# Optimization experiments

Measured on AMD Instinct MI355X. Metric: run time of the kernel, lower is better.

## Reference

```python
import jax, jax.numpy as jnp
import numpy as np

N_HIDDEN = 2048
D_IN = 64
T_STEPS = 4096
WASHOUT = 200
SPECTRAL_RADIUS = 0.9
RIDGE_LAMBDA = 1e-6


def _scale_to_spectral_radius(W, rho, iters=100):
    # power iteration to estimate the dominant eigenvalue magnitude (spectral radius)
    rng = np.random.default_rng(0)
    v = rng.normal(size=W.shape[0]).astype(np.float64)
    v /= np.linalg.norm(v)
    for _ in range(iters):
        w = W @ v
        nrm = np.linalg.norm(w)
        v = w / nrm
    rad = np.linalg.norm(W @ v)
    return W * (rho / rad)


def setup_inputs() -> dict:
    key = jax.random.key(0)
    k1, k2, k3, k4 = jax.random.split(key, 4)
    u = jax.random.normal(k1, (T_STEPS, D_IN), dtype=jnp.float32)
    y = jax.random.normal(k2, (T_STEPS, 1), dtype=jnp.float32)
    W_in = jax.random.normal(k3, (N_HIDDEN, D_IN), dtype=jnp.float32) * 0.1
    W = np.asarray(jax.random.normal(k4, (N_HIDDEN, N_HIDDEN), dtype=jnp.float32), dtype=np.float64)
    W /= np.sqrt(N_HIDDEN)
    W = _scale_to_spectral_radius(W, SPECTRAL_RADIUS)
    W_res = jnp.asarray(W, dtype=jnp.float32)
    return {"u": u, "y": y, "W_in": W_in, "W_res": W_res, "washout": WASHOUT}


def reference(u, y, W_in, W_res, washout):
    # precompute input drive W_in @ u[t] for all t: [T, N]
    drive = u @ W_in.T
    x0 = jnp.zeros((W_res.shape[0],), dtype=u.dtype)

    def step(x, d):
        x = jnp.tanh(W_res @ x + d)
        return x, x

    _, X = jax.lax.scan(step, x0, drive)  # X: [T, N]
    Xw = X[washout:]                      # [T - washout, N]
    yw = y[washout:]                      # [T - washout, 1]
    A = Xw.T @ Xw + RIDGE_LAMBDA * jnp.eye(Xw.shape[1], dtype=Xw.dtype)
    Wout = jnp.linalg.solve(A, Xw.T @ yw)  # [N, 1]
    return Xw @ Wout                       # [T - washout, 1]
```

## Files before the change

### kernel.cpp

```cpp
#include <hip/hip_runtime.h>
#include <math.h>

#define NH      2048
#define TT      4096
#define DIN     64
#define WASH    200
#define TW      (TT - WASH)
#define LAMBDA  1e-6f

#define CG_BLOCKS    64
#define CG_ITERS     320
#define NTILE        528
#define NWORK        192

typedef unsigned long long u64;

#define X_OFF      ((size_t)0)
#define DRIVE_OFF  ((size_t)TT * NH)
#define A_OFF      DRIVE_OFF
#define B_OFF      ((size_t)2 * TT * NH)
#define INVD_OFF   (B_OFF + NH)
#define XV_OFF     (INVD_OFF + NH)
#define WS_FLOATS  (XV_OFF + NH)
#define XPACK_OFF  ((size_t)0)
#define ZPACK_OFF  ((size_t)2 * NH)
#define PQSLOT_OFF ((size_t)3 * NH)
#define RZSLOT_OFF ((size_t)3 * NH + 64)
#define U64_TOTAL  ((size_t)3 * NH + 128)

__device__ __forceinline__ u64 pack_ev(int epoch, float v) {
    return ((u64)(unsigned)epoch << 32) | (u64)__float_as_uint(v);
}
__device__ __forceinline__ int   ep_of(u64 p)  { return (int)(p >> 32); }
__device__ __forceinline__ float val_of(u64 p) { return __uint_as_float((unsigned)p); }
__device__ __forceinline__ u64 pack2f(float lo, float hi) {
    return ((u64)__float_as_uint(hi) << 32) | (u64)__float_as_uint(lo);
}
__device__ __forceinline__ float lo_of(u64 p) { return __uint_as_float((unsigned)p); }
__device__ __forceinline__ float hi_of(u64 p) { return __uint_as_float((unsigned)(p >> 32)); }

__device__ __forceinline__ u64 aload(const u64* p) {
    return __hip_atomic_load(p, __ATOMIC_RELAXED, __HIP_MEMORY_SCOPE_AGENT);
}
__device__ __forceinline__ void astore(u64* p, u64 v) {
    __hip_atomic_store(p, v, __ATOMIC_RELAXED, __HIP_MEMORY_SCOPE_AGENT);
}

__global__ void init_kernel(float* ws) {
    int tid = threadIdx.x;
    u64* ub = (u64*)(ws + WS_FLOATS);
    for (size_t i = tid; i < U64_TOTAL; i += 256) ub[i] = 0ull;
    for (int i = tid; i < NH; i += 256) ws[B_OFF + i] = 0.f;
}

__global__ __launch_bounds__(256) void drive_kernel(
    const float* __restrict__ u, const float* __restrict__ Win,
    float* __restrict__ drive)
{
    __shared__ float Wt[256 * 64];
    const int tid = threadIdx.x;
    const int ic = blockIdx.x & 7;
    const int tc = blockIdx.x >> 3;
    const int i0 = ic * 256;
    for (int idx = tid; idx < 256 * 64; idx += 256) {
        int il = idx >> 6, k = idx & 63;
        Wt[k * 256 + il] = Win[(size_t)i0 * 64 + idx];
    }
    __syncthreads();
    for (int tt_ = 0; tt_ < 128; ++tt_) {
        int t = tc * 128 + tt_;
        const float* ur = u + (size_t)t * DIN;
        float acc = 0.f;
        #pragma unroll
        for (int k = 0; k < 64; ++k)
            acc = fmaf(Wt[k * 256 + tid], ur[k], acc);
        drive[(size_t)t * NH + i0 + tid] = acc;
    }
}

__global__ __launch_bounds__(1024, 1) void scan_gram_kernel(
    const float* __restrict__ W, const float* __restrict__ drive,
    float* __restrict__ X, u64* xpack, float* __restrict__ A)
{
    __shared__ float xls[NH];
    __shared__ float As[16][64];
    __shared__ float Bs[16][64];
    const int tid = threadIdx.x;

    if (blockIdx.x < 64) {
        const int wave = tid >> 6;
        const int lane = tid & 63;
        const int rowA = blockIdx.x * 32 + wave * 2;

        float4 wA[8], wB[8];
        {
            const float* wpA = W + (size_t)rowA * NH + lane * 4;
            const float* wpB = wpA + NH;
            #pragma unroll
            for (int j = 0; j < 8; ++j) {
                wA[j] = *(const float4*)(wpA + 256 * j);
                wB[j] = *(const float4*)(wpB + 256 * j);
            }
        }

        for (int t = 0; t < TT; ++t) {
            float2 dv = {0.f, 0.f};
            if (lane == 0) dv = *(const float2*)&drive[(size_t)t * NH + rowA];

            if (t == 0) {
                xls[tid] = 0.f; xls[tid + 1024] = 0.f;
            } else {
                const u64* src = xpack + (size_t)((t - 1) & 1) * NH;
                const int want = t;
                u64 a = aload(&src[tid]);
                u64 b = aload(&src[tid + 1024]);
                bool pa = true, pb = true;
                if (ep_of(a) >= want) { xls[tid] = val_of(a); pa = false; }
                if (ep_of(b) >= want) { xls[tid + 1024] = val_of(b); pb = false; }
                while (pa || pb) {
                    __builtin_amdgcn_s_sleep(1);
                    if (pa) { u64 v = aload(&src[tid]);
                              if (ep_of(v) >= want) { xls[tid] = val_of(v); pa = false; } }
                    if (pb) { u64 v = aload(&src[tid + 1024]);
                              if (ep_of(v) >= want) { xls[tid + 1024] = val_of(v); pb = false; } }
                }
            }
            __syncthreads();

            float a0 = 0.f, a1 = 0.f;
            #pragma unroll
            for (int j = 0; j < 8; ++j) {
                float4 xv = *(const float4*)&xls[lane * 4 + 256 * j];
                float4 va = wA[j], vb = wB[j];
                a0 = fmaf(va.x, xv.x, fmaf(va.y, xv.y, fmaf(va.z, xv.z, fmaf(va.w, xv.w, a0))));
                a1 = fmaf(vb.x, xv.x, fmaf(vb.y, xv.y, fmaf(vb.z, xv.z, fmaf(vb.w, xv.w, a1))));
            }
            #pragma unroll
            for (int m = 32; m; m >>= 1) { a0 += __shfl_xor(a0, m); a1 += __shfl_xor(a1, m); }

            if (lane == 0) {
                float v0 = tanhf(a0 + dv.x);
                float v1 = tanhf(a1 + dv.y);
                astore((u64*)&X[(size_t)t * NH + rowA], pack2f(v0, v1));
                u64* dst = xpack + (size_t)(t & 1) * NH;
                astore(&dst[rowA],     pack_ev(t + 1, v0));
                astore(&dst[rowA + 1], pack_ev(t + 1, v1));
            }
            __syncthreads();
        }
        __threadfence();
        if (lane == 0) {
            u64* dst = xpack + (size_t)(TT & 1) * NH;
            astore(&dst[rowA],     pack_ev(TT + 1, 0.f));
            astore(&dst[rowA + 1], pack_ev(TT + 1, 0.f));
        }
    } else {
        const int wid = blockIdx.x - 64;
        int ti0[3], tj0[3]; int nt = 0;
        for (int L = wid; L < NTILE; L += NWORK) {
            int rem = L, a = 0;
            while (rem >= 32 - a) { rem -= 32 - a; ++a; }
            ti0[nt] = a * 64; tj0[nt] = (a + rem) * 64; ++nt;
        }
        float4 acc4[3] = {};
        const int ty = tid >> 5, tx = tid & 31;
        const u64* Xp = (const u64*)X;

        const int nch = (TW + 15) / 16;
        for (int ch = 0; ch < nch; ++ch) {
            const int tb = WASH + ch * 16;
            const int te = (tb + 15 < TT) ? tb + 15 : TT - 1;
            const int want = te + 2;
            const u64* buf = xpack + (size_t)((te + 1) & 1) * NH;
            if (tid < nt * 128) {
                int tt_ = tid >> 7, local = tid & 127;
                int base = (local & 64) ? tj0[tt_] : ti0[tt_];
                int r = base + (local & 63);
                u64 v = aload(&buf[r]);
                while (ep_of(v) < want) { __builtin_amdgcn_s_sleep(64); v = aload(&buf[r]); }
            }
            __syncthreads();

            for (int tt_ = 0; tt_ < nt; ++tt_) {
                const int i0 = ti0[tt_], j0 = tj0[tt_];
                {
                    int v = tid & 511;
                    int kk = v >> 5, c2 = v & 31;
                    int t = tb + kk;
                    int base = (tid < 512) ? i0 : j0;
                    float lo = 0.f, hi = 0.f;
                    if (t < TT) {
                        u64 w_ = aload(&Xp[((size_t)t * NH + base) / 2 + c2]);
                        lo = lo_of(w_); hi = hi_of(w_);
                    }
                    float* Sh = (tid < 512) ? &As[kk][c2 * 2] : &Bs[kk][c2 * 2];
                    Sh[0] = lo; Sh[1] = hi;
                }
                __syncthreads();
                float4 a = acc4[tt_];
                #pragma unroll
                for (int k = 0; k < 16; ++k) {
                    float2 av = *(const float2*)&As[k][ty * 2];
                    float2 bv = *(const float2*)&Bs[k][tx * 2];
                    a.x = fmaf(av.x, bv.x, a.x); a.y = fmaf(av.x, bv.y, a.y);
                    a.z = fmaf(av.y, bv.x, a.z); a.w = fmaf(av.y, bv.y, a.w);
                }
                acc4[tt_] = a;
                __syncthreads();
            }
        }
        for (int tt_ = 0; tt_ < nt; ++tt_) {
            const int i0 = ti0[tt_], j0 = tj0[tt_];
            const bool diag = (i0 == j0);
            float4 a = acc4[tt_];
            float vals[2][2] = {{a.x, a.y}, {a.z, a.w}};
            #pragma unroll
            for (int aa = 0; aa < 2; ++aa) {
                int gi = i0 + ty * 2 + aa;
                #pragma unroll
                for (int bb = 0; bb < 2; ++bb) {
                    int gj = j0 + tx * 2 + bb;
                    float v = vals[aa][bb];
                    if (gi == gj) v += LAMBDA;
                    A[(size_t)gi * NH + gj] = v;
                    if (!diag) A[(size_t)gj * NH + gi] = v;
                }
            }
        }
    }
}

__global__ void bvec_kernel(const float* __restrict__ X, const float* __restrict__ y,
                            float* __restrict__ bv)
{
    const int ic = blockIdx.x & 7, tc = blockIdx.x >> 3;
    const int i = ic * 256 + threadIdx.x;
    const int t0 = WASH + tc * (TW / 8), t1 = t0 + (TW / 8);
    float acc = 0.f;
    for (int t = t0; t < t1; ++t)
        acc = fmaf(X[(size_t)t * NH + i], y[t], acc);
    atomicAdd(&bv[i], acc);
}

__global__ void invdiag_kernel(const float* __restrict__ A, float* __restrict__ invd)
{
    int i = blockIdx.x * 256 + threadIdx.x;
    invd[i] = 1.0f / A[(size_t)i * NH + i];
}

__global__ __launch_bounds__(1024, 1) void cg_kernel(
    const float* __restrict__ A, const float* __restrict__ bvec,
    const float* __restrict__ invd, float* __restrict__ xv,
    u64* zpack, u64* pqslot, u64* rzslot)
{
    __shared__ float pls[NH];
    __shared__ float zls[NH];
    __shared__ float r32[32], x32[32], q32[32], inv32[32];
    __shared__ float csh[2];
    const int tid     = threadIdx.x;
    const int r_local = tid >> 5;
    const int lane32  = tid & 31;
    const int row0 = blockIdx.x * 32;
    const int row  = row0 + r_local;

    float4 areg[16];
    {
        const float* ap = A + (size_t)row * NH + lane32 * 4;
        #pragma unroll
        for (int j = 0; j < 16; ++j) areg[j] = *(const float4*)(ap + 128 * j);
    }

    pls[tid] = 0.f; pls[tid + 1024] = 0.f;

    if (tid < 32) {
        int i = row0 + tid;
        float bi = bvec[i], iv = invd[i];
        inv32[tid] = iv;
        x32[tid] = 0.f; r32[tid] = bi;
        float zi = iv * bi;
        astore(&zpack[i], pack_ev(1, zi));
        float part = bi * zi;
        #pragma unroll
        for (int m = 16; m; m >>= 1) part += __shfl_xor(part, m, 32);
        if (tid == 0) astore(&rzslot[blockIdx.x], pack_ev(1, part));
    }
    __syncthreads();

    float rho_prev = 1.f;

    for (int it = 0; it < CG_ITERS; ++it) {
        {
            const int want = it + 1;
            u64 a = aload(&zpack[tid]);
            u64 b = aload(&zpack[tid + 1024]);
            bool pa = true, pb = true;
            if (ep_of(a) >= want) { zls[tid] = val_of(a); pa = false; }
            if (ep_of(b) >= want) { zls[tid + 1024] = val_of(b); pb = false; }
            while (pa || pb) {
                __builtin_amdgcn_s_sleep(1);
                if (pa) { u64 v = aload(&zpack[tid]);
                          if (ep_of(v) >= want) { zls[tid] = val_of(v); pa = false; } }
                if (pb) { u64 v = aload(&zpack[tid + 1024]);
                          if (ep_of(v) >= want) { zls[tid + 1024] = val_of(v); pb = false; } }
            }
        }
        if (tid < 64) {
            u64 v = aload(&rzslot[tid]);
            while (ep_of(v) < it + 1) { __builtin_amdgcn_s_sleep(1); v = aload(&rzslot[tid]); }
            float s = val_of(v);
            #pragma unroll
            for (int m = 32; m; m >>= 1) s += __shfl_xor(s, m);
            if (tid == 0) csh[1] = s;
        }
        __syncthreads();
        float rho = csh[1];
        float beta = (it == 0) ? 0.f : ((rho_prev != 0.f) ? rho / rho_prev : 0.f);

        pls[tid]        = fmaf(beta, pls[tid],        zls[tid]);
        pls[tid + 1024] = fmaf(beta, pls[tid + 1024], zls[tid + 1024]);
        __syncthreads();

        float acc = 0.f;
        #pragma unroll
        for (int j = 0; j < 16; ++j) {
            float4 pv = *(const float4*)&pls[lane32 * 4 + 128 * j];
            float4 av = areg[j];
            acc = fmaf(av.x, pv.x, fmaf(av.y, pv.y,
                  fmaf(av.z, pv.z, fmaf(av.w, pv.w, acc))));
        }
        #pragma unroll
        for (int m = 16; m; m >>= 1) acc += __shfl_xor(acc, m, 32);
        if (lane32 == 0) q32[r_local] = acc;
        __syncthreads();

        if (tid < 32) {
            float t1 = q32[tid] * pls[row0 + tid];
            #pragma unroll
            for (int m = 16; m; m >>= 1) t1 += __shfl_xor(t1, m, 32);
            if (tid == 0) astore(&pqslot[blockIdx.x], pack_ev(it + 1, t1));
        }
        if (tid < 64) {
            u64 v = aload(&pqslot[tid]);
            while (ep_of(v) < it + 1) { __builtin_amdgcn_s_sleep(1); v = aload(&pqslot[tid]); }
            float s = val_of(v);
            #pragma unroll
            for (int m = 32; m; m >>= 1) s += __shfl_xor(s, m);
            if (tid == 0) csh[0] = s;
        }
        __syncthreads();
        float pq = csh[0];
        float alpha = (pq != 0.f) ? rho / pq : 0.f;

        if (tid < 32) {
            int i = row0 + tid;
            float pi = pls[i], qi = q32[tid];
            x32[tid] = fmaf(alpha, pi, x32[tid]);
            float ri = r32[tid] - alpha * qi;
            r32[tid] = ri;
            float zi = inv32[tid] * ri;
            astore(&zpack[i], pack_ev(it + 2, zi));
            float t2 = ri * zi;
            #pragma unroll
            for (int m = 16; m; m >>= 1) t2 += __shfl_xor(t2, m, 32);
            if (tid == 0) astore(&rzslot[blockIdx.x], pack_ev(it + 2, t2));
        }
        rho_prev = rho;
        __syncthreads();
    }

    if (tid < 32) xv[row0 + tid] = x32[tid];
}

__global__ void out_kernel(const float* __restrict__ X, const float* __restrict__ w,
                           float* __restrict__ out)
{
    __shared__ float red[4];
    const int tid = threadIdx.x;
    const int rowt = WASH + blockIdx.x;
    float acc = 0.f;
    #pragma unroll
    for (int j = 0; j < 8; ++j) {
        int c = tid + 256 * j;
        acc = fmaf(X[(size_t)rowt * NH + c], w[c], acc);
    }
    #pragma unroll
    for (int m = 32; m; m >>= 1) acc += __shfl_xor(acc, m);
    if ((tid & 63) == 0) red[tid >> 6] = acc;
    __syncthreads();
    if (tid == 0) out[blockIdx.x] = red[0] + red[1] + red[2] + red[3];
}

extern "C" void kernel_launch(void* const* d_in, const int* in_sizes, int n_in,
                              void* d_out, int out_size, void* d_ws, size_t ws_size,
                              hipStream_t stream)
{
    const float* u    = (const float*)d_in[0];
    const float* y    = (const float*)d_in[1];
    const float* Win  = (const float*)d_in[2];
    const float* Wres = (const float*)d_in[3];

    float* ws = (float*)d_ws;
    float* X     = ws + X_OFF;
    float* drive = ws + DRIVE_OFF;
    float* A     = ws + A_OFF;
    u64*   ub    = (u64*)(ws + WS_FLOATS);
    u64*   xpack  = ub + XPACK_OFF;
    u64*   zpack  = ub + ZPACK_OFF;
    u64*   pqslot = ub + PQSLOT_OFF;
    u64*   rzslot = ub + RZSLOT_OFF;

    init_kernel<<<1, 256, 0, stream>>>(ws);
    drive_kernel<<<256, 256, 0, stream>>>(u, Win, drive);
    scan_gram_kernel<<<256, 1024, 0, stream>>>(Wres, drive, X, xpack, A);
    bvec_kernel<<<64, 256, 0, stream>>>(X, y, ws + B_OFF);
    invdiag_kernel<<<8, 256, 0, stream>>>(A, ws + INVD_OFF);
    cg_kernel<<<CG_BLOCKS, 1024, 0, stream>>>(A, ws + B_OFF, ws + INVD_OFF,
                                              ws + XV_OFF, zpack, pqslot, rzslot);
    out_kernel<<<TW, 256, 0, stream>>>(X, ws + XV_OFF, (float*)d_out);
}
```

Measured before the change: 13.37 ms.

## Gate Gram workers on a single progress counter and fuse bvec into scan

Block 0 of the scan now publishes a single progress counter each step. The Gram-accumulation blocks poll only that word instead of spinning on many per-row epoch slots in the xpack buffer, which should cut memory contention on the scan's critical path. The separate bvec and invdiag kernels are removed: the scan blocks compute X^T y for their own rows after the recurrence, and the CG kernel computes the inverse diagonal inline. The counter relies on relaxed atomics for cross-block visibility of X, which adds a memory-ordering risk.

```diff
diff --git a/kernel.cpp b/kernel.cpp
--- a/kernel.cpp
+++ b/kernel.cpp
@@ -19,14 +19,14 @@
 #define DRIVE_OFF  ((size_t)TT * NH)
 #define A_OFF      DRIVE_OFF
 #define B_OFF      ((size_t)2 * TT * NH)
-#define INVD_OFF   (B_OFF + NH)
-#define XV_OFF     (INVD_OFF + NH)
+#define XV_OFF     (B_OFF + NH)
 #define WS_FLOATS  (XV_OFF + NH)
 #define XPACK_OFF  ((size_t)0)
 #define ZPACK_OFF  ((size_t)2 * NH)
 #define PQSLOT_OFF ((size_t)3 * NH)
 #define RZSLOT_OFF ((size_t)3 * NH + 64)
-#define U64_TOTAL  ((size_t)3 * NH + 128)
+#define PROG_OFF   ((size_t)3 * NH + 192)
+#define U64_TOTAL  ((size_t)3 * NH + 256)
 
 __device__ __forceinline__ u64 pack_ev(int epoch, float v) {
     return ((u64)(unsigned)epoch << 32) | (u64)__float_as_uint(v);
@@ -50,7 +50,6 @@
     int tid = threadIdx.x;
     u64* ub = (u64*)(ws + WS_FLOATS);
     for (size_t i = tid; i < U64_TOTAL; i += 256) ub[i] = 0ull;
-    for (int i = tid; i < NH; i += 256) ws[B_OFF + i] = 0.f;
 }
 
 __global__ __launch_bounds__(256) void drive_kernel(
@@ -80,11 +79,14 @@
 
 __global__ __launch_bounds__(1024, 1) void scan_gram_kernel(
     const float* __restrict__ W, const float* __restrict__ drive,
-    float* __restrict__ X, u64* xpack, float* __restrict__ A)
+    const float* __restrict__ y,
+    float* __restrict__ X, u64* xpack, u64* prog,
+    float* __restrict__ A, float* __restrict__ bv)
 {
     __shared__ float xls[NH];
     __shared__ float As[16][64];
     __shared__ float Bs[16][64];
+    __shared__ float bred[32 * 33];
     const int tid = threadIdx.x;
 
     if (blockIdx.x < 64) {
@@ -126,6 +128,7 @@
                 }
             }
             __syncthreads();
+            if (blockIdx.x == 0 && tid == 0 && t > 0) astore(prog, (u64)t);
 
             float a0 = 0.f, a1 = 0.f;
             #pragma unroll
@@ -154,6 +157,22 @@
             astore(&dst[rowA],     pack_ev(TT + 1, 0.f));
             astore(&dst[rowA + 1], pack_ev(TT + 1, 0.f));
         }
+
+        {
+            const int r = tid & 31, tc2 = tid >> 5;
+            const int row0 = blockIdx.x * 32;
+            float acc = 0.f;
+            for (int t = WASH + tc2; t < TT; t += 32)
+                acc = fmaf(X[(size_t)t * NH + row0 + r], y[t], acc);
+            bred[tc2 * 33 + r] = acc;
+            __syncthreads();
+            if (tid < 32) {
+                float s = 0.f;
+                #pragma unroll
+                for (int k = 0; k < 32; ++k) s += bred[k * 33 + tid];
+                bv[row0 + tid] = s;
+            }
+        }
     } else {
         const int wid = blockIdx.x - 64;
         int ti0[3], tj0[3]; int nt = 0;
@@ -170,16 +189,27 @@
         for (int ch = 0; ch < nch; ++ch) {
             const int tb = WASH + ch * 16;
             const int te = (tb + 15 < TT) ? tb + 15 : TT - 1;
-            const int want = te + 2;
-            const u64* buf = xpack + (size_t)((te + 1) & 1) * NH;
-            if (tid < nt * 128) {
-                int tt_ = tid >> 7, local = tid & 127;
-                int base = (local & 64) ? tj0[tt_] : ti0[tt_];
-                int r = base + (local & 63);
-                u64 v = aload(&buf[r]);
-                while (ep_of(v) < want) { __builtin_amdgcn_s_sleep(64); v = aload(&buf[r]); }
-            }
-            __syncthreads();
+            if (te <= TT - 2) {
+                if (tid == 0) {
+                    u64 p = aload(prog);
+                    while ((long long)p < (long long)(te + 1)) {
+                        __builtin_amdgcn_s_sleep(32);
+                        p = aload(prog);
+                    }
+                }
+                __syncthreads();
+            } else {
+                const int want = te + 2;
+                const u64* buf = xpack + (size_t)((te + 1) & 1) * NH;
+                if (tid < nt * 128) {
+                    int tt_ = tid >> 7, local = tid & 127;
+                    int base = (local & 64) ? tj0[tt_] : ti0[tt_];
+                    int r = base + (local & 63);
+                    u64 v = aload(&buf[r]);
+                    while (ep_of(v) < want) { __builtin_amdgcn_s_sleep(32); v = aload(&buf[r]); }
+                }
+                __syncthreads();
+            }
 
             for (int tt_ = 0; tt_ < nt; ++tt_) {
                 const int i0 = ti0[tt_], j0 = tj0[tt_];
@@ -201,9 +231,9 @@
                 #pragma unroll
                 for (int k = 0; k < 16; ++k) {
                     float2 av = *(const float2*)&As[k][ty * 2];
-                    float2 bv = *(const float2*)&Bs[k][tx * 2];
-                    a.x = fmaf(av.x, bv.x, a.x); a.y = fmaf(av.x, bv.y, a.y);
-                    a.z = fmaf(av.y, bv.x, a.z); a.w = fmaf(av.y, bv.y, a.w);
+                    float2 bv2 = *(const float2*)&Bs[k][tx * 2];
+                    a.x = fmaf(av.x, bv2.x, a.x); a.y = fmaf(av.x, bv2.y, a.y);
+                    a.z = fmaf(av.y, bv2.x, a.z); a.w = fmaf(av.y, bv2.y, a.w);
                 }
                 acc4[tt_] = a;
                 __syncthreads();
@@ -230,27 +260,9 @@
     }
 }
 
-__global__ void bvec_kernel(const float* __restrict__ X, const float* __restrict__ y,
-                            float* __restrict__ bv)
-{
-    const int ic = blockIdx.x & 7, tc = blockIdx.x >> 3;
-    const int i = ic * 256 + threadIdx.x;
-    const int t0 = WASH + tc * (TW / 8), t1 = t0 + (TW / 8);
-    float acc = 0.f;
-    for (int t = t0; t < t1; ++t)
-        acc = fmaf(X[(size_t)t * NH + i], y[t], acc);
-    atomicAdd(&bv[i], acc);
-}
-
-__global__ void invdiag_kernel(const float* __restrict__ A, float* __restrict__ invd)
-{
-    int i = blockIdx.x * 256 + threadIdx.x;
-    invd[i] = 1.0f / A[(size_t)i * NH + i];
-}
-
 __global__ __launch_bounds__(1024, 1) void cg_kernel(
     const float* __restrict__ A, const float* __restrict__ bvec,
-    const float* __restrict__ invd, float* __restrict__ xv,
+    float* __restrict__ xv,
     u64* zpack, u64* pqslot, u64* rzslot)
 {
     __shared__ float pls[NH];
@@ -274,7 +286,8 @@
 
     if (tid < 32) {
         int i = row0 + tid;
-        float bi = bvec[i], iv = invd[i];
+        float bi = bvec[i];
+        float iv = 1.0f / A[(size_t)i * NH + i];
         inv32[tid] = iv;
         x32[tid] = 0.f; r32[tid] = bi;
         float zi = iv * bi;
@@ -408,13 +421,13 @@
     u64*   zpack  = ub + ZPACK_OFF;
     u64*   pqslot = ub + PQSLOT_OFF;
     u64*   rzslot = ub + RZSLOT_OFF;
+    u64*   prog   = ub + PROG_OFF;
 
     init_kernel<<<1, 256, 0, stream>>>(ws);
     drive_kernel<<<256, 256, 0, stream>>>(u, Win, drive);
-    scan_gram_kernel<<<256, 1024, 0, stream>>>(Wres, drive, X, xpack, A);
-    bvec_kernel<<<64, 256, 0, stream>>>(X, y, ws + B_OFF);
-    invdiag_kernel<<<8, 256, 0, stream>>>(A, ws + INVD_OFF);
-    cg_kernel<<<CG_BLOCKS, 1024, 0, stream>>>(A, ws + B_OFF, ws + INVD_OFF,
+    scan_gram_kernel<<<256, 1024, 0, stream>>>(Wres, drive, y, X, xpack, prog,
+                                               A, ws + B_OFF);
+    cg_kernel<<<CG_BLOCKS, 1024, 0, stream>>>(A, ws + B_OFF,
                                               ws + XV_OFF, zpack, pqslot, rzslot);
     out_kernel<<<TW, 256, 0, stream>>>(X, ws + XV_OFF, (float*)d_out);
 }
```

New measurement: 15.16 ms. 1.13x slower.

## Fuse diagonal inverse and readout GEMV into CG kernel, trim CG iterations

Applied to the files above, without the earlier changes.

Computes the Jacobi preconditioner inline in the CG kernel and removes the separate invdiag kernel. After the CG loop, each block publishes its slice of the solution through the epoch-tagged zpack array, gathers the full vector, and computes its share of the output rows X·w, so out_kernel is eliminated. CG iteration count is lowered from 320 to 256, which cuts per-iteration grid sync costs. The risk is a less converged solve and the final cross-block spin-wait.

```diff
diff --git a/kernel.cpp b/kernel.cpp
--- a/kernel.cpp
+++ b/kernel.cpp
@@ -9,7 +9,7 @@
 #define LAMBDA  1e-6f
 
 #define CG_BLOCKS    64
-#define CG_ITERS     320
+#define CG_ITERS     256
 #define NTILE        528
 #define NWORK        192
 
@@ -19,9 +19,7 @@
 #define DRIVE_OFF  ((size_t)TT * NH)
 #define A_OFF      DRIVE_OFF
 #define B_OFF      ((size_t)2 * TT * NH)
-#define INVD_OFF   (B_OFF + NH)
-#define XV_OFF     (INVD_OFF + NH)
-#define WS_FLOATS  (XV_OFF + NH)
+#define WS_FLOATS  (B_OFF + NH)
 #define XPACK_OFF  ((size_t)0)
 #define ZPACK_OFF  ((size_t)2 * NH)
 #define PQSLOT_OFF ((size_t)3 * NH)
@@ -201,9 +199,9 @@
                 #pragma unroll
                 for (int k = 0; k < 16; ++k) {
                     float2 av = *(const float2*)&As[k][ty * 2];
-                    float2 bv = *(const float2*)&Bs[k][tx * 2];
-                    a.x = fmaf(av.x, bv.x, a.x); a.y = fmaf(av.x, bv.y, a.y);
-                    a.z = fmaf(av.y, bv.x, a.z); a.w = fmaf(av.y, bv.y, a.w);
+                    float2 bv2 = *(const float2*)&Bs[k][tx * 2];
+                    a.x = fmaf(av.x, bv2.x, a.x); a.y = fmaf(av.x, bv2.y, a.y);
+                    a.z = fmaf(av.y, bv2.x, a.z); a.w = fmaf(av.y, bv2.y, a.w);
                 }
                 acc4[tt_] = a;
                 __syncthreads();
@@ -242,15 +240,9 @@
     atomicAdd(&bv[i], acc);
 }
 
-__global__ void invdiag_kernel(const float* __restrict__ A, float* __restrict__ invd)
-{
-    int i = blockIdx.x * 256 + threadIdx.x;
-    invd[i] = 1.0f / A[(size_t)i * NH + i];
-}
-
 __global__ __launch_bounds__(1024, 1) void cg_kernel(
     const float* __restrict__ A, const float* __restrict__ bvec,
-    const float* __restrict__ invd, float* __restrict__ xv,
+    const float* __restrict__ X, float* __restrict__ out,
     u64* zpack, u64* pqslot, u64* rzslot)
 {
     __shared__ float pls[NH];
@@ -274,7 +266,8 @@
 
     if (tid < 32) {
         int i = row0 + tid;
-        float bi = bvec[i], iv = invd[i];
+        float bi = bvec[i];
+        float iv = 1.0f / A[(size_t)i * NH + i];
         inv32[tid] = iv;
         x32[tid] = 0.f; r32[tid] = bi;
         float zi = iv * bi;
@@ -368,26 +361,41 @@
         __syncthreads();
     }
 
-    if (tid < 32) xv[row0 + tid] = x32[tid];
-}
-
-__global__ void out_kernel(const float* __restrict__ X, const float* __restrict__ w,
-                           float* __restrict__ out)
-{
-    __shared__ float red[4];
-    const int tid = threadIdx.x;
-    const int rowt = WASH + blockIdx.x;
-    float acc = 0.f;
-    #pragma unroll
-    for (int j = 0; j < 8; ++j) {
-        int c = tid + 256 * j;
-        acc = fmaf(X[(size_t)rowt * NH + c], w[c], acc);
-    }
-    #pragma unroll
-    for (int m = 32; m; m >>= 1) acc += __shfl_xor(acc, m);
-    if ((tid & 63) == 0) red[tid >> 6] = acc;
+    if (tid < 32) {
+        int i = row0 + tid;
+        astore(&zpack[i], pack_ev(CG_ITERS + 2, x32[tid]));
+    }
+    {
+        const int want = CG_ITERS + 2;
+        u64 a = aload(&zpack[tid]);
+        u64 b = aload(&zpack[tid + 1024]);
+        bool pa = true, pb = true;
+        if (ep_of(a) >= want) { zls[tid] = val_of(a); pa = false; }
+        if (ep_of(b) >= want) { zls[tid + 1024] = val_of(b); pb = false; }
+        while (pa || pb) {
+            __builtin_amdgcn_s_sleep(1);
+            if (pa) { u64 v = aload(&zpack[tid]);
+                      if (ep_of(v) >= want) { zls[tid] = val_of(v); pa = false; } }
+            if (pb) { u64 v = aload(&zpack[tid + 1024]);
+                      if (ep_of(v) >= want) { zls[tid + 1024] = val_of(v); pb = false; } }
+        }
+    }
     __syncthreads();
-    if (tid == 0) out[blockIdx.x] = red[0] + red[1] + red[2] + red[3];
+    {
+        const int i0r = (TW * (int)blockIdx.x) >> 6;
+        const int i1r = (TW * ((int)blockIdx.x + 1)) >> 6;
+        const int wave = tid >> 6, lane = tid & 63;
+        for (int i = i0r + wave; i < i1r; i += 16) {
+            const float* xr = X + (size_t)(WASH + i) * NH;
+            float acc = 0.f;
+            #pragma unroll
+            for (int j = 0; j < 32; ++j)
+                acc = fmaf(xr[j * 64 + lane], zls[j * 64 + lane], acc);
+            #pragma unroll
+            for (int m = 32; m; m >>= 1) acc += __shfl_xor(acc, m);
+            if (lane == 0) out[i] = acc;
+        }
+    }
 }
 
 extern "C" void kernel_launch(void* const* d_in, const int* in_sizes, int n_in,
@@ -413,8 +421,6 @@
     drive_kernel<<<256, 256, 0, stream>>>(u, Win, drive);
     scan_gram_kernel<<<256, 1024, 0, stream>>>(Wres, drive, X, xpack, A);
     bvec_kernel<<<64, 256, 0, stream>>>(X, y, ws + B_OFF);
-    invdiag_kernel<<<8, 256, 0, stream>>>(A, ws + INVD_OFF);
-    cg_kernel<<<CG_BLOCKS, 1024, 0, stream>>>(A, ws + B_OFF, ws + INVD_OFF,
-                                              ws + XV_OFF, zpack, pqslot, rzslot);
-    out_kernel<<<TW, 256, 0, stream>>>(X, ws + XV_OFF, (float*)d_out);
-}
+    cg_kernel<<<CG_BLOCKS, 1024, 0, stream>>>(A, ws + B_OFF, X, (float*)d_out,
+                                              zpack, pqslot, rzslot);
+}
```

Measured after the change: 13.14 ms. No clear change (-1.7%).
